# Performance work log

Measured on AMD Instinct MI355X. Metric: run time of the kernel, lower is better.

## Reference

```python
import jax, jax.numpy as jnp
import numpy as np

C = 1.0                 # Poincare ball curvature
PROJ_EPS = 1e-5         # boundary epsilon for projection
ACOSH_EPS = 1e-7        # numerical floor for arccosh argument


def setup_inputs() -> dict:
    key = jax.random.key(0)
    k1, k2 = jax.random.split(key)
    num_tokens, embed_dim = 30522, 64
    batch, seq = 4, 1024
    token_ids = jax.random.randint(k1, (batch, seq), 0, num_tokens, dtype=jnp.int64)
    weight = jax.random.normal(k2, (num_tokens, embed_dim), dtype=jnp.float32) * 0.05
    scale = jnp.asarray(0.5, dtype=jnp.float32)
    return {"token_ids": token_ids, "weight": weight, "scale": scale}


def _poincare_bias(token_ids, weight, scale):
    ids = jnp.clip(token_ids, 0, weight.shape[0] - 1)
    emb = weight[ids]                                   # (b, s, d)
    # project onto the Poincare ball: clip norm to (1 - eps) / sqrt(c)
    sqc = jnp.sqrt(C)
    max_norm = (1.0 - PROJ_EPS) / sqc
    norm = jnp.linalg.norm(emb, axis=-1, keepdims=True)
    emb = jnp.where(norm > max_norm, emb * (max_norm / jnp.maximum(norm, 1e-12)), emb)
    # pairwise hyperbolic distance via arccosh form (== Mobius-add/artanh form):
    # d(x,y) = (1/sqrt(c)) * arccosh(1 + 2c||x-y||^2 / ((1-c||x||^2)(1-c||y||^2)))
    x2 = jnp.sum(emb * emb, axis=-1)                    # (b, s)
    gram = jnp.einsum("bid,bjd->bij", emb, emb)        # (b, s, s)
    sqdist = jnp.maximum(x2[:, :, None] + x2[:, None, :] - 2.0 * gram, 0.0)
    denom = (1.0 - C * x2)[:, :, None] * (1.0 - C * x2)[:, None, :]
    arg = 1.0 + 2.0 * C * sqdist / denom
    dist = jnp.arccosh(jnp.maximum(arg, 1.0 + ACOSH_EPS)) / sqc
    return scale * -dist                                # (b, s, s)


def reference(token_ids, weight, scale):
    return _poincare_bias(token_ids, weight, scale)
```

## Files before the change

kernel.cpp:

```cpp
#include <hip/hip_runtime.h>
#include <hip/hip_bf16.h>

typedef __attribute__((ext_vector_type(8)))  short bf16x8;
typedef __attribute__((ext_vector_type(4)))  float f32x4;
typedef __attribute__((ext_vector_type(16))) float f32x16;

#define EMB_DIM 64
#define LDS_STRIDE 72

__global__ __launch_bounds__(256) void project_kernel(
    const int* __restrict__ ids, const float* __restrict__ weight,
    short* __restrict__ E, float* __restrict__ x2g, int n_tok, int vocab)
{
    const int gt = blockIdx.x * 256 + threadIdx.x;
    const int r  = gt >> 1;
    const int h2 = gt & 1;
    if (r >= n_tok) return;

    int id = ids[r];
    id = min(max(id, 0), vocab - 1);

    const f32x4* W = (const f32x4*)(weight + (size_t)id * EMB_DIM + h2 * 32);
    f32x4 v[8];
    #pragma unroll
    for (int k = 0; k < 8; ++k) v[k] = W[k];

    float s = 0.f;
    #pragma unroll
    for (int k = 0; k < 8; ++k)
        s += v[k].x * v[k].x + v[k].y * v[k].y + v[k].z * v[k].z + v[k].w * v[k].w;
    s += __shfl_xor(s, 1);

    const float max_norm = 0.99999f;
    float nrm = sqrtf(s);
    float mul = (nrm > max_norm) ? (max_norm / fmaxf(nrm, 1e-12f)) : 1.f;

    const float* vf = (const float*)v;
    bf16x8 hv[4];
    float s2 = 0.f;
    #pragma unroll
    for (int k = 0; k < 32; ++k) {
        __hip_bfloat16 hb = __float2bfloat16(vf[k] * mul);
        float hf = __bfloat162float(hb);
        s2 += hf * hf;
        hv[k >> 3][k & 7] = __builtin_bit_cast(short, hb);
    }
    s2 += __shfl_xor(s2, 1);

    bf16x8* dst = (bf16x8*)(E + (size_t)r * EMB_DIM + h2 * 32);
    #pragma unroll
    for (int k = 0; k < 4; ++k) dst[k] = hv[k];
    if (h2 == 0) x2g[r] = s2;
}

__global__ __launch_bounds__(256) void bias_kernel(
    const short* __restrict__ E, const float* __restrict__ x2g,
    const float* __restrict__ scale_p, float* __restrict__ out, int S)
{
    __shared__ short Es[128 * LDS_STRIDE];
    __shared__ float x2s[128];

    const int b  = blockIdx.z;
    const int i0 = blockIdx.y * 64;
    const int j0 = blockIdx.x * 64;
    const int t  = threadIdx.x;

    {
        const int r    = t >> 1;
        const int h2   = t & 1;
        const int lrow = (r < 64) ? (i0 + r) : (j0 + r - 64);
        const size_t erow = (size_t)b * S + lrow;

        const bf16x8* src = (const bf16x8*)(E + erow * EMB_DIM + h2 * 32);
        short* dst = Es + r * LDS_STRIDE + h2 * 32;
        #pragma unroll
        for (int k = 0; k < 4; ++k) ((bf16x8*)dst)[k] = src[k];
        if (h2 == 0) x2s[r] = x2g[erow];
    }
    __syncthreads();

    const int wid  = t >> 6;
    const int lane = t & 63;
    const int m  = lane & 31;
    const int h  = lane >> 5;
    const int ia = (wid >> 1) * 32;
    const int jb = (wid & 1) * 32;

    const short* Ear = Es + (ia + m) * LDS_STRIDE + h * 8;
    const short* Ebr = Es + (64 + jb + m) * LDS_STRIDE + h * 8;

    f32x16 acc = {};
    #pragma unroll
    for (int kb = 0; kb < 4; ++kb) {
        bf16x8 av = *(const bf16x8*)(Ear + kb * 16);
        bf16x8 bv = *(const bf16x8*)(Ebr + kb * 16);
        acc = __builtin_amdgcn_mfma_f32_32x32x16_bf16(av, bv, acc, 0, 0, 0);
    }

    const float xj    = x2s[64 + jb + m];
    const float scale = scale_p[0];
    const float omxj  = 1.f - xj;

    float* O = out + ((size_t)b * S + i0 + ia + 4 * h) * S + j0 + jb + m;

    #pragma unroll
    for (int g = 0; g < 4; ++g) {
        f32x4 xi4 = *(const f32x4*)(x2s + ia + g * 8 + 4 * h);
        #pragma unroll
        for (int e = 0; e < 4; ++e) {
            float gv = acc[g * 4 + e];
            float xi = xi4[e];
            float sq  = fmaxf(xi + xj - 2.f * gv, 0.f);
            float den = (1.f - xi) * omxj;
            float u = fmaxf(2.f * sq * __builtin_amdgcn_rcpf(den), 1.1920929e-7f);
            float w = 1.f + u + __builtin_amdgcn_sqrtf(u * (u + 2.f));
            float dist = 0.69314718056f * __builtin_amdgcn_logf(w);
            __builtin_nontemporal_store(-scale * dist, &O[(size_t)(g * 8 + e) * S]);
        }
    }
}

__global__ __launch_bounds__(256) void fused_bias_kernel(
    const int* __restrict__ ids, const float* __restrict__ weight,
    const float* __restrict__ scale_p, float* __restrict__ out,
    int S, int vocab)
{
    __shared__ short Es[128 * LDS_STRIDE];
    __shared__ float x2s[128];

    const int b  = blockIdx.z;
    const int i0 = blockIdx.y * 64;
    const int j0 = blockIdx.x * 64;
    const int t  = threadIdx.x;

    {
        const int r  = t >> 1;
        const int h2 = t & 1;
        const int grow = (r < 64) ? (i0 + r) : (j0 + r - 64);
        int id = ids[(size_t)b * S + grow];
        id = min(max(id, 0), vocab - 1);

        const f32x4* W = (const f32x4*)(weight + (size_t)id * EMB_DIM + h2 * 32);
        f32x4 v[8];
        #pragma unroll
        for (int k = 0; k < 8; ++k) v[k] = W[k];

        float s = 0.f;
        #pragma unroll
        for (int k = 0; k < 8; ++k)
            s += v[k].x * v[k].x + v[k].y * v[k].y + v[k].z * v[k].z + v[k].w * v[k].w;
        s += __shfl_xor(s, 1);

        const float max_norm = 0.99999f;
        float nrm = sqrtf(s);
        float mul = (nrm > max_norm) ? (max_norm / fmaxf(nrm, 1e-12f)) : 1.f;

        const float* vf = (const float*)v;
        bf16x8 hv[4];
        float s2 = 0.f;
        #pragma unroll
        for (int k = 0; k < 32; ++k) {
            __hip_bfloat16 hb = __float2bfloat16(vf[k] * mul);
            float hf = __bfloat162float(hb);
            s2 += hf * hf;
            hv[k >> 3][k & 7] = __builtin_bit_cast(short, hb);
        }
        s2 += __shfl_xor(s2, 1);

        short* dst = Es + r * LDS_STRIDE + h2 * 32;
        #pragma unroll
        for (int k = 0; k < 4; ++k)
            *(bf16x8*)(dst + k * 8) = hv[k];
        if (h2 == 0) x2s[r] = s2;
    }
    __syncthreads();

    const int wid  = t >> 6;
    const int lane = t & 63;
    const int m  = lane & 31;
    const int h  = lane >> 5;
    const int ia = (wid >> 1) * 32;
    const int jb = (wid & 1) * 32;

    const short* Ear = Es + (ia + m) * LDS_STRIDE + h * 8;
    const short* Ebr = Es + (64 + jb + m) * LDS_STRIDE + h * 8;

    f32x16 acc = {};
    #pragma unroll
    for (int kb = 0; kb < 4; ++kb) {
        bf16x8 av = *(const bf16x8*)(Ear + kb * 16);
        bf16x8 bv = *(const bf16x8*)(Ebr + kb * 16);
        acc = __builtin_amdgcn_mfma_f32_32x32x16_bf16(av, bv, acc, 0, 0, 0);
    }

    const float xj    = x2s[64 + jb + m];
    const float scale = scale_p[0];
    const float omxj  = 1.f - xj;

    float* O = out + ((size_t)b * S + i0 + ia + 4 * h) * S + j0 + jb + m;

    #pragma unroll
    for (int g = 0; g < 4; ++g) {
        f32x4 xi4 = *(const f32x4*)(x2s + ia + g * 8 + 4 * h);
        #pragma unroll
        for (int e = 0; e < 4; ++e) {
            float gv = acc[g * 4 + e];
            float xi = xi4[e];
            float sq  = fmaxf(xi + xj - 2.f * gv, 0.f);
            float den = (1.f - xi) * omxj;
            float u = fmaxf(2.f * sq * __builtin_amdgcn_rcpf(den), 1.1920929e-7f);
            float w = 1.f + u + __builtin_amdgcn_sqrtf(u * (u + 2.f));
            float dist = 0.69314718056f * __builtin_amdgcn_logf(w);
            O[(size_t)(g * 8 + e) * S] = -scale * dist;
        }
    }
}

extern "C" void kernel_launch(void* const* d_in, const int* in_sizes, int n_in,
                              void* d_out, int out_size, void* d_ws, size_t ws_size,
                              hipStream_t stream) {
    const int*   ids     = (const int*)d_in[0];
    const float* weight  = (const float*)d_in[1];
    const float* scale_p = (const float*)d_in[2];
    float*       out     = (float*)d_out;

    const int n_tok = in_sizes[0];
    const int vocab = in_sizes[1] / EMB_DIM;
    const int S     = out_size / n_tok;
    const int B     = n_tok / S;

    const size_t needE = (size_t)n_tok * EMB_DIM * sizeof(short);
    const size_t needX = (size_t)n_tok * sizeof(float);

    if (d_ws != nullptr && ws_size >= needE + needX) {
        short* E   = (short*)d_ws;
        float* x2g = (float*)((char*)d_ws + needE);

        dim3 g1((unsigned)((n_tok * 2 + 255) / 256));
        project_kernel<<<g1, 256, 0, stream>>>(ids, weight, E, x2g, n_tok, vocab);

        dim3 grid(S / 64, S / 64, B);
        bias_kernel<<<grid, 256, 0, stream>>>(E, x2g, scale_p, out, S);
    } else {
        dim3 grid(S / 64, S / 64, B);
        fused_bias_kernel<<<grid, 256, 0, stream>>>(ids, weight, scale_p, out, S, vocab);
    }
}
```

Baseline: 71.85 us.

## Enlarge bias tile to 128x128 and precompute reciprocal norms per token

The bias kernel now uses 128x128 output tiles with 1024-thread blocks, so each staged embedding row feeds twice as many outputs. The projection kernel also writes 1/(1-||x||^2) per token, which replaces the per-element reciprocal of the product denominator with two multiplies, and the scale and log constant are folded into one coefficient. The projection kernel moves to 64-thread blocks. In exchange, LDS use grows and occupancy per CU falls, the workspace must hold one more float array, and the fast path now requires S to be a multiple of 128.

```diff
diff --git a/kernel.cpp b/kernel.cpp
--- a/kernel.cpp
+++ b/kernel.cpp
@@ -8,11 +8,12 @@
 #define EMB_DIM 64
 #define LDS_STRIDE 72
 
-__global__ __launch_bounds__(256) void project_kernel(
+__global__ __launch_bounds__(64) void project_kernel(
     const int* __restrict__ ids, const float* __restrict__ weight,
-    short* __restrict__ E, float* __restrict__ x2g, int n_tok, int vocab)
+    short* __restrict__ E, float* __restrict__ x2g, float* __restrict__ rxg,
+    int n_tok, int vocab)
 {
-    const int gt = blockIdx.x * 256 + threadIdx.x;
+    const int gt = blockIdx.x * 64 + threadIdx.x;
     const int r  = gt >> 1;
     const int h2 = gt & 1;
     if (r >= n_tok) return;
@@ -50,32 +51,38 @@
     bf16x8* dst = (bf16x8*)(E + (size_t)r * EMB_DIM + h2 * 32);
     #pragma unroll
     for (int k = 0; k < 4; ++k) dst[k] = hv[k];
-    if (h2 == 0) x2g[r] = s2;
-}
-
-__global__ __launch_bounds__(256) void bias_kernel(
+    if (h2 == 0) {
+        x2g[r] = s2;
+        rxg[r] = 1.0f / (1.0f - s2);
+    }
+}
+
+__global__ __launch_bounds__(1024) void bias_kernel(
     const short* __restrict__ E, const float* __restrict__ x2g,
-    const float* __restrict__ scale_p, float* __restrict__ out, int S)
+    const float* __restrict__ rxg, const float* __restrict__ scale_p,
+    float* __restrict__ out, int S)
 {
-    __shared__ short Es[128 * LDS_STRIDE];
-    __shared__ float x2s[128];
+    __shared__ short Es[256 * LDS_STRIDE];
+    __shared__ float x2s[256];
+    __shared__ float rxs[256];
 
     const int b  = blockIdx.z;
-    const int i0 = blockIdx.y * 64;
-    const int j0 = blockIdx.x * 64;
+    const int i0 = blockIdx.y * 128;
+    const int j0 = blockIdx.x * 128;
     const int t  = threadIdx.x;
 
     {
-        const int r    = t >> 1;
-        const int h2   = t & 1;
-        const int lrow = (r < 64) ? (i0 + r) : (j0 + r - 64);
+        const int r    = t >> 2;
+        const int qd   = t & 3;
+        const int lrow = (r < 128) ? (i0 + r) : (j0 + r - 128);
         const size_t erow = (size_t)b * S + lrow;
 
-        const bf16x8* src = (const bf16x8*)(E + erow * EMB_DIM + h2 * 32);
-        short* dst = Es + r * LDS_STRIDE + h2 * 32;
-        #pragma unroll
-        for (int k = 0; k < 4; ++k) ((bf16x8*)dst)[k] = src[k];
-        if (h2 == 0) x2s[r] = x2g[erow];
+        const bf16x8* src = (const bf16x8*)(E + erow * EMB_DIM + qd * 16);
+        short* dst = Es + r * LDS_STRIDE + qd * 16;
+        ((bf16x8*)dst)[0] = src[0];
+        ((bf16x8*)dst)[1] = src[1];
+        if (qd == 0)      x2s[r] = x2g[erow];
+        else if (qd == 1) rxs[r] = rxg[erow];
     }
     __syncthreads();
 
@@ -83,11 +90,11 @@
     const int lane = t & 63;
     const int m  = lane & 31;
     const int h  = lane >> 5;
-    const int ia = (wid >> 1) * 32;
-    const int jb = (wid & 1) * 32;
+    const int ia = (wid >> 2) * 32;
+    const int jb = (wid & 3) * 32;
 
     const short* Ear = Es + (ia + m) * LDS_STRIDE + h * 8;
-    const short* Ebr = Es + (64 + jb + m) * LDS_STRIDE + h * 8;
+    const short* Ebr = Es + (128 + jb + m) * LDS_STRIDE + h * 8;
 
     f32x16 acc = {};
     #pragma unroll
@@ -97,25 +104,25 @@
         acc = __builtin_amdgcn_mfma_f32_32x32x16_bf16(av, bv, acc, 0, 0, 0);
     }
 
-    const float xj    = x2s[64 + jb + m];
-    const float scale = scale_p[0];
-    const float omxj  = 1.f - xj;
+    const float xj   = x2s[128 + jb + m];
+    const float rxj2 = 2.0f * rxs[128 + jb + m];
+    const float c1   = scale_p[0] * -0.69314718056f;
 
     float* O = out + ((size_t)b * S + i0 + ia + 4 * h) * S + j0 + jb + m;
 
     #pragma unroll
     for (int g = 0; g < 4; ++g) {
         f32x4 xi4 = *(const f32x4*)(x2s + ia + g * 8 + 4 * h);
+        f32x4 rx4 = *(const f32x4*)(rxs + ia + g * 8 + 4 * h);
         #pragma unroll
         for (int e = 0; e < 4; ++e) {
             float gv = acc[g * 4 + e];
             float xi = xi4[e];
-            float sq  = fmaxf(xi + xj - 2.f * gv, 0.f);
-            float den = (1.f - xi) * omxj;
-            float u = fmaxf(2.f * sq * __builtin_amdgcn_rcpf(den), 1.1920929e-7f);
-            float w = 1.f + u + __builtin_amdgcn_sqrtf(u * (u + 2.f));
-            float dist = 0.69314718056f * __builtin_amdgcn_logf(w);
-            __builtin_nontemporal_store(-scale * dist, &O[(size_t)(g * 8 + e) * S]);
+            float sq = fmaxf(xi + xj - 2.f * gv, 0.f);
+            float u  = fmaxf(sq * (rx4[e] * rxj2), 1.1920929e-7f);
+            float w  = 1.f + u + __builtin_amdgcn_sqrtf(u * (u + 2.f));
+            float r  = c1 * __builtin_amdgcn_logf(w);
+            __builtin_nontemporal_store(r, &O[(size_t)(g * 8 + e) * S]);
         }
     }
 }
@@ -232,15 +239,16 @@
     const size_t needE = (size_t)n_tok * EMB_DIM * sizeof(short);
     const size_t needX = (size_t)n_tok * sizeof(float);
 
-    if (d_ws != nullptr && ws_size >= needE + needX) {
+    if (d_ws != nullptr && ws_size >= needE + 2 * needX && (S % 128) == 0) {
         short* E   = (short*)d_ws;
         float* x2g = (float*)((char*)d_ws + needE);
-
-        dim3 g1((unsigned)((n_tok * 2 + 255) / 256));
-        project_kernel<<<g1, 256, 0, stream>>>(ids, weight, E, x2g, n_tok, vocab);
-
-        dim3 grid(S / 64, S / 64, B);
-        bias_kernel<<<grid, 256, 0, stream>>>(E, x2g, scale_p, out, S);
+        float* rxg = (float*)((char*)d_ws + needE + needX);
+
+        dim3 g1((unsigned)((n_tok * 2 + 63) / 64));
+        project_kernel<<<g1, 64, 0, stream>>>(ids, weight, E, x2g, rxg, n_tok, vocab);
+
+        dim3 grid(S / 128, S / 128, B);
+        bias_kernel<<<grid, 1024, 0, stream>>>(E, x2g, rxg, scale_p, out, S);
     } else {
         dim3 grid(S / 64, S / 64, B);
         fused_bias_kernel<<<grid, 256, 0, stream>>>(ids, weight, scale_p, out, S, vocab);
```

After: 72.08 us. About the same (+0.3%).
